# Optimization experiments

Measured on AMD Instinct MI355X. Metric: run time of the kernel, lower is better.

## Reference

```python
import jax, jax.numpy as jnp
import numpy as np

D_MODEL = 1024
NUM_HEADS = 16
D_K = D_MODEL // NUM_HEADS
B, S = 2, 2048


def setup_inputs() -> dict:
    key = jax.random.key(0)
    ks = jax.random.split(key, 11)
    sc = 1.0 / np.sqrt(D_MODEL)
    return {
        "Q_input": jax.random.normal(ks[0], (B, S, D_MODEL), jnp.float32),
        "K_input": jax.random.normal(ks[1], (B, S, D_MODEL), jnp.float32),
        "V_input": jax.random.normal(ks[2], (B, S, D_MODEL), jnp.float32),
        "Wq": jax.random.normal(ks[3], (D_MODEL, D_MODEL), jnp.float32) * sc,
        "bq": jax.random.normal(ks[4], (D_MODEL,), jnp.float32) * 0.01,
        "Wk": jax.random.normal(ks[5], (D_MODEL, D_MODEL), jnp.float32) * sc,
        "bk": jax.random.normal(ks[6], (D_MODEL,), jnp.float32) * 0.01,
        "Wv": jax.random.normal(ks[7], (D_MODEL, D_MODEL), jnp.float32) * sc,
        "bv": jax.random.normal(ks[8], (D_MODEL,), jnp.float32) * 0.01,
        "Wo": jax.random.normal(ks[9], (D_MODEL, D_MODEL), jnp.float32) * sc,
        "bo": jax.random.normal(ks[10], (D_MODEL,), jnp.float32) * 0.01,
    }


def reference(Q_input, K_input, V_input, Wq, bq, Wk, bk, Wv, bv, Wo, bo):
    # Linear projections (torch Linear: x @ W.T + b)
    Q = Q_input @ Wq.T + bq  # [B,S,D]
    K = K_input @ Wk.T + bk
    V = V_input @ Wv.T + bv
    # split heads -> [B,H,S,dk]
    def split(x):
        return x.reshape(B, S, NUM_HEADS, D_K).transpose(0, 2, 1, 3)
    Qh, Kh, Vh = split(Q), split(K), split(V)
    scale = 1.0 / jnp.sqrt(jnp.asarray(D_K, Qh.dtype))
    scores = jnp.einsum('bhqd,bhkd->bhqk', Qh, Kh) * scale  # [B,H,S,S]
    attn = jax.nn.softmax(scores, axis=-1)
    ctx = jnp.einsum('bhqk,bhkd->bhqd', attn, Vh)  # [B,H,S,dk]
    concat = ctx.transpose(0, 2, 1, 3).reshape(B, S, D_MODEL)
    out = concat @ Wo.T + bo  # dropout is identity in eval
    return out
```

## Files before the change

### kernel.cpp

```cpp
#include <hip/hip_runtime.h>
#include <stdint.h>

#define DM   1024
#define NH   16
#define DKH  64
#define BBATCH 2
#define SEQ  2048
#define MTOK (BBATCH*SEQ)

typedef unsigned short u16;
typedef __attribute__((ext_vector_type(8))) short  bf16x8;
typedef __attribute__((ext_vector_type(4))) float  f32x4;

struct PtrArr11 { const void* p[11]; };
struct U16Arr11 { u16* p[11]; };

__device__ __forceinline__ float bf2f(u16 u) {
  union { unsigned int i; float f; } z; z.i = ((unsigned int)u) << 16; return z.f;
}
__device__ __forceinline__ u16 f2bf(float f) {
  union { float f; unsigned int i; } z; z.f = f;
  unsigned int i = z.i + 0x7fffu + ((z.i >> 16) & 1u);
  return (u16)(i >> 16);
}
__device__ __forceinline__ unsigned pack2bf(float lo, float hi) {
  union { float f; unsigned int i; } a, b; a.f = lo; b.f = hi;
  return ((a.i + 0x8000u) >> 16) | (((b.i + 0x8000u) >> 16) << 16);
}

__device__ __forceinline__ void gld16(const void* g, void* l) {
  __builtin_amdgcn_global_load_lds(
      (const __attribute__((address_space(1))) void*)g,
      (__attribute__((address_space(3))) void*)l,
      16, 0, 0);
}

__global__ void k_detect(const unsigned int* __restrict__ w, int* __restrict__ flag) {
  const int ln = threadIdx.x & 63;
  const unsigned int word = w[ln];
  const unsigned int ex = (word >> 7) & 0xFFu;
  const int hit = (ex >= 100u && ex <= 126u) ? 1 : 0;
  unsigned long long m = __ballot(hit);
  if (ln == 0) *flag = (__popcll(m) >= 40) ? 0 : 1;
}

__global__ __launch_bounds__(256) void k_convert_all(PtrArr11 src, U16Arr11 dst,
                                                     const int* __restrict__ flag) {
  if (*flag == 0) return;
  const int b = blockIdx.x;
  int seg, base;
  if      (b <  2048) { seg = 0;  base = 0;    }
  else if (b <  4096) { seg = 1;  base = 2048; }
  else if (b <  6144) { seg = 2;  base = 4096; }
  else if (b <  6656) { seg = 3;  base = 6144; }
  else if (b == 6656) { seg = 4;  base = 6656; }
  else if (b <  7169) { seg = 5;  base = 6657; }
  else if (b == 7169) { seg = 6;  base = 7169; }
  else if (b <  7682) { seg = 7;  base = 7170; }
  else if (b == 7682) { seg = 8;  base = 7682; }
  else if (b <  8195) { seg = 9;  base = 7683; }
  else                { seg = 10; base = 8195; }
  const int n = (seg < 3) ? (MTOK * DM) : ((seg & 1) ? (DM * DM) : DM);
  const int i0 = (b - base) * 2048 + threadIdx.x * 8;
  if (i0 >= n) return;
  const float* s = (const float*)src.p[seg] + i0;
  bf16x8 o;
#pragma unroll
  for (int j = 0; j < 8; ++j) o[j] = (short)f2bf(s[j]);
  *(bf16x8*)(dst.p[seg] + i0) = o;
}

__device__ __forceinline__ void gemm_body(const u16* __restrict__ X,
                                          const u16* __restrict__ W,
                                          const u16* __restrict__ bias,
                                          void* __restrict__ out,
                                          int isf32out)
{
  __shared__ __attribute__((aligned(16))) u16 sA[128 * 32];
  __shared__ __attribute__((aligned(16))) u16 sB[128 * 32];
  const int tid = threadIdx.x;
  const int ln = tid & 63, wv = tid >> 6;
  const int wm = wv & 1, wn = wv >> 1;
  const int m0 = blockIdx.y * 128, n0 = blockIdx.x * 128;
  const int fr = ln & 15, fq = ln >> 4;
  const int srow = ln >> 2, sslot = (ln & 3) * 8;

  f32x4 acc[4][4];
#pragma unroll
  for (int i = 0; i < 4; ++i)
#pragma unroll
    for (int j = 0; j < 4; ++j) acc[i][j] = (f32x4){0.f, 0.f, 0.f, 0.f};

  const u16* pA = X + (size_t)(m0 + wv * 32 + srow) * DM + sslot;
  const u16* pB = W + (size_t)(n0 + wv * 32 + srow) * DM + sslot;
  u16* lA0 = sA + (wv * 2) * 512; u16* lA1 = sA + (wv * 2 + 1) * 512;
  u16* lB0 = sB + (wv * 2) * 512; u16* lB1 = sB + (wv * 2 + 1) * 512;

  for (int k0 = 0; k0 < DM; k0 += 32) {
    gld16(pA + k0,            lA0);
    gld16(pA + 16 * DM + k0,  lA1);
    gld16(pB + k0,            lB0);
    gld16(pB + 16 * DM + k0,  lB1);
    asm volatile("s_waitcnt vmcnt(0)" ::: "memory");
    __syncthreads();

    bf16x8 af[4], bfg[4];
#pragma unroll
    for (int t = 0; t < 4; ++t) {
      af[t]  = *(const bf16x8*)(sA + (wm * 64 + t * 16 + fr) * 32 + fq * 8);
      bfg[t] = *(const bf16x8*)(sB + (wn * 64 + t * 16 + fr) * 32 + fq * 8);
    }
#pragma unroll
    for (int i = 0; i < 4; ++i)
#pragma unroll
      for (int j = 0; j < 4; ++j)
        acc[i][j] = __builtin_amdgcn_mfma_f32_16x16x32_bf16(af[i], bfg[j], acc[i][j], 0, 0, 0);
    __syncthreads();
  }

#pragma unroll
  for (int i = 0; i < 4; ++i) {
    const int row = m0 + wm * 64 + i * 16 + fq * 4;
#pragma unroll
    for (int j = 0; j < 4; ++j) {
      const int col = n0 + wn * 64 + j * 16 + fr;
      const float bv = bf2f(bias[col]);
#pragma unroll
      for (int r = 0; r < 4; ++r) {
        const float val = acc[i][j][r] + bv;
        const size_t idx = (size_t)(row + r) * DM + col;
        if (isf32out) ((float*)out)[idx] = val;
        else          ((u16*)out)[idx]   = f2bf(val);
      }
    }
  }
}

__global__ __launch_bounds__(256, 2) void k_gemm_qkv(
    PtrArr11 orig, U16Arr11 conv, const int* __restrict__ flag,
    u16* oq, u16* ok, u16* ov)
{
  const int f = *flag;
  const int z = blockIdx.z;
  const u16* X  = f ? conv.p[z]         : (const u16*)orig.p[z];
  const u16* W  = f ? conv.p[3 + 2 * z] : (const u16*)orig.p[3 + 2 * z];
  const u16* bi = f ? conv.p[4 + 2 * z] : (const u16*)orig.p[4 + 2 * z];
  u16* o = (z == 0) ? oq : (z == 1) ? ok : ov;
  gemm_body(X, W, bi, o, 0);
}

__global__ __launch_bounds__(256, 2) void k_gemm_one(
    const u16* X, const void* Wo_o, const u16* Wo_c,
    const void* bo_o, const u16* bo_c, const int* __restrict__ flag, void* o)
{
  const int f = *flag;
  const u16* W  = f ? Wo_c : (const u16*)Wo_o;
  const u16* bi = f ? bo_c : (const u16*)bo_o;
  gemm_body(X, W, bi, o, f);
}

__global__ __launch_bounds__(256) void k_transpose(const u16* __restrict__ in,
                                                   u16* __restrict__ out)
{
  __shared__ u16 t[64][66];
  const int b = blockIdx.z;
  const int s0 = blockIdx.x * 64, d0 = blockIdx.y * 64;
  const int c = threadIdx.x & 63, r0 = threadIdx.x >> 6;
#pragma unroll
  for (int i = 0; i < 16; ++i) {
    const int r = r0 + 4 * i;
    t[r][c] = in[(size_t)(b * SEQ + s0 + r) * DM + d0 + c];
  }
  __syncthreads();
#pragma unroll
  for (int i = 0; i < 16; ++i) {
    const int r = r0 + 4 * i;
    out[(size_t)(b * DM + d0 + r) * SEQ + s0 + c] = t[c][r];
  }
}

__global__ __launch_bounds__(256, 2) void k_attn(
    const u16* __restrict__ Qp, const u16* __restrict__ Kp,
    const u16* __restrict__ Vt, u16* __restrict__ ctx)
{
  __shared__ __attribute__((aligned(16))) u16 sK[64 * 72];
  __shared__ __attribute__((aligned(16))) u16 sV[64 * 72];

  const int tid = threadIdx.x;
  const int ln = tid & 63, wv = tid >> 6;
  const int bh = blockIdx.y;
  const int b = bh >> 4, h = bh & 15;
  const int q0 = blockIdx.x * 128 + wv * 32;
  const int fr = ln & 15, fq = ln >> 4;
  const int str = tid >> 2, stq = (tid & 3) * 16;

  const int addr0 = 4 * (fr + 16 * ((fq & 1) * 2));
  const int addr1 = addr0 + 64;

  bf16x8 qf[2][2];
#pragma unroll
  for (int mt = 0; mt < 2; ++mt)
#pragma unroll
    for (int ks = 0; ks < 2; ++ks) {
      const u16* src = Qp + (size_t)(b * SEQ + q0 + mt * 16 + fr) * DM + h * DKH + ks * 32 + fq * 8;
      bf16x8 v = *(const bf16x8*)src;
      bf16x8 w;
#pragma unroll
      for (int j = 0; j < 8; ++j)
        w[j] = (short)f2bf(bf2f((u16)v[j]) * 0.125f);
      qf[mt][ks] = w;
    }

  float l_acc[2] = {0.f, 0.f};
  f32x4 o_acc[2][4];
#pragma unroll
  for (int mt = 0; mt < 2; ++mt)
#pragma unroll
    for (int dt = 0; dt < 4; ++dt) o_acc[mt][dt] = (f32x4){0.f, 0.f, 0.f, 0.f};

  for (int kb = 0; kb < SEQ / 64; ++kb) {
    const int key0 = kb * 64;
    {
      const u16* gK = Kp + (size_t)(b * SEQ + key0 + str) * DM + h * DKH + stq;
      const u16* gV = Vt + (size_t)(b * DM + h * DKH + str) * SEQ + key0 + stq;
      *(bf16x8*)(sK + str * 72 + stq)     = *(const bf16x8*)gK;
      *(bf16x8*)(sK + str * 72 + stq + 8) = *(const bf16x8*)(gK + 8);
      *(bf16x8*)(sV + str * 72 + stq)     = *(const bf16x8*)gV;
      *(bf16x8*)(sV + str * 72 + stq + 8) = *(const bf16x8*)(gV + 8);
    }
    __syncthreads();

    bf16x8 kf[4][2];
#pragma unroll
    for (int kt = 0; kt < 4; ++kt)
#pragma unroll
      for (int ks = 0; ks < 2; ++ks)
        kf[kt][ks] = *(const bf16x8*)(sK + (kt * 16 + fr) * 72 + ks * 32 + fq * 8);

    bf16x8 vf[4][2];
#pragma unroll
    for (int dt = 0; dt < 4; ++dt)
#pragma unroll
      for (int ks = 0; ks < 2; ++ks)
        vf[dt][ks] = *(const bf16x8*)(sV + (dt * 16 + fr) * 72 + ks * 32 + fq * 8);

#pragma unroll
    for (int mt = 0; mt < 2; ++mt) {
      f32x4 s2[4];
#pragma unroll
      for (int kt = 0; kt < 4; ++kt) s2[kt] = (f32x4){0.f, 0.f, 0.f, 0.f};
#pragma unroll
      for (int kt = 0; kt < 4; ++kt)
#pragma unroll
        for (int ks = 0; ks < 2; ++ks)
          s2[kt] = __builtin_amdgcn_mfma_f32_16x16x32_bf16(kf[kt][ks], qf[mt][ks], s2[kt], 0, 0, 0);

      unsigned pk[4][2];
#pragma unroll
      for (int kt = 0; kt < 4; ++kt) {
        float p0 = __expf(s2[kt][0]), p1 = __expf(s2[kt][1]);
        float p2 = __expf(s2[kt][2]), p3 = __expf(s2[kt][3]);
        l_acc[mt] += (p0 + p1) + (p2 + p3);
        pk[kt][0] = pack2bf(p0, p1);
        pk[kt][1] = pack2bf(p2, p3);
      }

      bf16x8 pb[2];
#pragma unroll
      for (int ks = 0; ks < 2; ++ks) {
        union { unsigned u[4]; bf16x8 v; } cv;
#pragma unroll
        for (int pp = 0; pp < 4; ++pp) {
          const int addr = (pp >> 1) ? addr1 : addr0;
          const int vlo = __builtin_amdgcn_ds_bpermute(addr, (int)pk[ks * 2][pp & 1]);
          const int vhi = __builtin_amdgcn_ds_bpermute(addr, (int)pk[ks * 2 + 1][pp & 1]);
          cv.u[pp] = (fq >= 2) ? (unsigned)vhi : (unsigned)vlo;
        }
        pb[ks] = cv.v;
      }

#pragma unroll
      for (int dt = 0; dt < 4; ++dt)
#pragma unroll
        for (int ks = 0; ks < 2; ++ks)
          o_acc[mt][dt] = __builtin_amdgcn_mfma_f32_16x16x32_bf16(vf[dt][ks], pb[ks], o_acc[mt][dt], 0, 0, 0);
    }

    __syncthreads();
  }

  float inv[2];
#pragma unroll
  for (int mt = 0; mt < 2; ++mt) {
    float l = l_acc[mt];
    l += __shfl_xor(l, 16);
    l += __shfl_xor(l, 32);
    inv[mt] = 1.0f / l;
  }

#pragma unroll
  for (int mt = 0; mt < 2; ++mt) {
    const int qrow = q0 + mt * 16 + fr;
#pragma unroll
    for (int dt = 0; dt < 4; ++dt)
#pragma unroll
      for (int r = 0; r < 4; ++r) {
        const int col = h * DKH + dt * 16 + fq * 4 + r;
        ctx[(size_t)(b * SEQ + qrow) * DM + col] = f2bf(o_acc[mt][dt][r] * inv[mt]);
      }
  }
}

extern "C" void kernel_launch(void* const* d_in, const int* in_sizes, int n_in,
                              void* d_out, int out_size, void* d_ws, size_t ws_size,
                              hipStream_t stream)
{
  char* ws = (char*)d_ws;
  int* flag = (int*)ws;

  const size_t TOKSZ = (size_t)MTOK * DM * sizeof(u16);
  const size_t WSZ   = (size_t)DM * DM * sizeof(u16);
  const size_t BSZ   = 4096;

  size_t off = 256;
  u16* Qc  = (u16*)(ws + off); off += TOKSZ;
  u16* Kc  = (u16*)(ws + off); off += TOKSZ;
  u16* Vc  = (u16*)(ws + off); off += TOKSZ;
  u16* Wqc = (u16*)(ws + off); off += WSZ;
  u16* Wkc = (u16*)(ws + off); off += WSZ;
  u16* Wvc = (u16*)(ws + off); off += WSZ;
  u16* Woc = (u16*)(ws + off); off += WSZ;
  u16* bqc = (u16*)(ws + off); off += BSZ;
  u16* bkc = (u16*)(ws + off); off += BSZ;
  u16* bvc = (u16*)(ws + off); off += BSZ;
  u16* boc = (u16*)(ws + off); off += BSZ;
  u16* Qp  = (u16*)(ws + off); off += TOKSZ;
  u16* Kp  = (u16*)(ws + off); off += TOKSZ;
  u16* Vp  = (u16*)(ws + off); off += TOKSZ;
  u16* Vt  = Qc;
  u16* ctx = Kc;

  PtrArr11 orig;
  for (int i = 0; i < 11; ++i) orig.p[i] = d_in[i];
  U16Arr11 conv;
  conv.p[0] = Qc;  conv.p[1] = Kc;  conv.p[2] = Vc;
  conv.p[3] = Wqc; conv.p[4] = bqc; conv.p[5] = Wkc; conv.p[6] = bkc;
  conv.p[7] = Wvc; conv.p[8] = bvc; conv.p[9] = Woc; conv.p[10] = boc;

  dim3 blk(256);

  k_detect<<<1, 64, 0, stream>>>((const unsigned int*)d_in[3], flag);
  k_convert_all<<<8196, blk, 0, stream>>>(orig, conv, flag);
  k_gemm_qkv<<<dim3(DM / 128, MTOK / 128, 3), blk, 0, stream>>>(
      orig, conv, flag, Qp, Kp, Vp);
  k_transpose<<<dim3(SEQ / 64, DM / 64, BBATCH), blk, 0, stream>>>(Vp, Vt);
  k_attn<<<dim3(SEQ / 128, BBATCH * NH), blk, 0, stream>>>(Qp, Kp, Vt, ctx);
  k_gemm_one<<<dim3(DM / 128, MTOK / 128, 1), blk, 0, stream>>>(
      ctx, d_in[9], Woc, d_in[10], boc, flag, d_out);
}
```

Baseline: 260.5 us.

## Restructure attention to 32x32 MFMA with split-K waves and LDS reduction

```diff
diff --git a/kernel.cpp b/kernel.cpp
--- a/kernel.cpp
+++ b/kernel.cpp
@@ -9,8 +9,10 @@
 #define MTOK (BBATCH*SEQ)
 
 typedef unsigned short u16;
-typedef __attribute__((ext_vector_type(8))) short  bf16x8;
-typedef __attribute__((ext_vector_type(4))) float  f32x4;
+typedef __attribute__((ext_vector_type(8)))  short bf16x8;
+typedef __attribute__((ext_vector_type(4)))  float f32x4;
+typedef __attribute__((ext_vector_type(16))) float f32x16;
+typedef __attribute__((ext_vector_type(2)))  unsigned uint2v;
 
 struct PtrArr11 { const void* p[11]; };
 struct U16Arr11 { u16* p[11]; };
@@ -27,6 +29,31 @@
   union { float f; unsigned int i; } a, b; a.f = lo; b.f = hi;
   return ((a.i + 0x8000u) >> 16) | (((b.i + 0x8000u) >> 16) << 16);
 }
+__device__ __forceinline__ unsigned pack2bf_rne(float lo, float hi) {
+  return (unsigned)f2bf(lo) | ((unsigned)f2bf(hi) << 16);
+}
+__device__ __forceinline__ f32x16 zero16() {
+  f32x16 z;
+#pragma unroll
+  for (int i = 0; i < 16; ++i) z[i] = 0.f;
+  return z;
+}
+
+#if __has_builtin(__builtin_amdgcn_permlane32_swap)
+__device__ __forceinline__ void half_swap(unsigned &a, unsigned &b) {
+  uint2v r = __builtin_amdgcn_permlane32_swap(a, b, false, false);
+  a = r[0]; b = r[1];
+}
+#else
+__device__ __forceinline__ void half_swap(unsigned &a, unsigned &b) {
+  unsigned ax = (unsigned)__shfl_xor((int)a, 32);
+  unsigned bx = (unsigned)__shfl_xor((int)b, 32);
+  const bool lo = (threadIdx.x & 63) < 32;
+  unsigned na = lo ? a : bx;
+  unsigned nb = lo ? ax : b;
+  a = na; b = nb;
+}
+#endif
 
 __device__ __forceinline__ void gld16(const void* g, void* l) {
   __builtin_amdgcn_global_load_lds(
@@ -136,7 +163,7 @@
   }
 }
 
-__global__ __launch_bounds__(256, 2) void k_gemm_qkv(
+__global__ __launch_bounds__(256, 3) void k_gemm_qkv(
     PtrArr11 orig, U16Arr11 conv, const int* __restrict__ flag,
     u16* oq, u16* ok, u16* ov)
 {
@@ -149,7 +176,7 @@
   gemm_body(X, W, bi, o, 0);
 }
 
-__global__ __launch_bounds__(256, 2) void k_gemm_one(
+__global__ __launch_bounds__(256, 3) void k_gemm_one(
     const u16* X, const void* Wo_o, const u16* Wo_c,
     const void* bo_o, const u16* bo_c, const int* __restrict__ flag, void* o)
 {
@@ -179,135 +206,157 @@
   }
 }
 
-__global__ __launch_bounds__(256, 2) void k_attn(
+__global__ __launch_bounds__(128, 2) void k_attn(
     const u16* __restrict__ Qp, const u16* __restrict__ Kp,
     const u16* __restrict__ Vt, u16* __restrict__ ctx)
 {
-  __shared__ __attribute__((aligned(16))) u16 sK[64 * 72];
-  __shared__ __attribute__((aligned(16))) u16 sV[64 * 72];
+  __shared__ __attribute__((aligned(16))) u16 lds[19456];
 
   const int tid = threadIdx.x;
   const int ln = tid & 63, wv = tid >> 6;
   const int bh = blockIdx.y;
   const int b = bh >> 4, h = bh & 15;
-  const int q0 = blockIdx.x * 128 + wv * 32;
-  const int fr = ln & 15, fq = ln >> 4;
-  const int str = tid >> 2, stq = (tid & 3) * 16;
-
-  const int addr0 = 4 * (fr + 16 * ((fq & 1) * 2));
-  const int addr1 = addr0 + 64;
-
-  bf16x8 qf[2][2];
-#pragma unroll
-  for (int mt = 0; mt < 2; ++mt)
-#pragma unroll
-    for (int ks = 0; ks < 2; ++ks) {
-      const u16* src = Qp + (size_t)(b * SEQ + q0 + mt * 16 + fr) * DM + h * DKH + ks * 32 + fq * 8;
+  const int q0 = blockIdx.x * 64;
+  const int m32 = ln & 31, half = ln >> 5;
+  const int srow = ln >> 3, schk = (ln & 7) * 8;
+
+  u16* sK = lds + wv * 9728;
+  u16* sV = sK + 4864;
+
+  bf16x8 qf[2][4];
+#pragma unroll
+  for (int qt = 0; qt < 2; ++qt)
+#pragma unroll
+    for (int ks = 0; ks < 4; ++ks) {
+      const u16* src = Qp + (size_t)(b * SEQ + q0 + qt * 32 + m32) * DM + h * DKH + ks * 16 + half * 8;
       bf16x8 v = *(const bf16x8*)src;
       bf16x8 w;
 #pragma unroll
       for (int j = 0; j < 8; ++j)
         w[j] = (short)f2bf(bf2f((u16)v[j]) * 0.125f);
-      qf[mt][ks] = w;
+      qf[qt][ks] = w;
     }
 
   float l_acc[2] = {0.f, 0.f};
-  f32x4 o_acc[2][4];
-#pragma unroll
-  for (int mt = 0; mt < 2; ++mt)
-#pragma unroll
-    for (int dt = 0; dt < 4; ++dt) o_acc[mt][dt] = (f32x4){0.f, 0.f, 0.f, 0.f};
-
-  for (int kb = 0; kb < SEQ / 64; ++kb) {
+  f32x16 o_acc[2][2];
+#pragma unroll
+  for (int qt = 0; qt < 2; ++qt)
+#pragma unroll
+    for (int dt = 0; dt < 2; ++dt) o_acc[qt][dt] = zero16();
+
+  for (int kb = wv; kb < SEQ / 64; kb += 2) {
     const int key0 = kb * 64;
-    {
-      const u16* gK = Kp + (size_t)(b * SEQ + key0 + str) * DM + h * DKH + stq;
-      const u16* gV = Vt + (size_t)(b * DM + h * DKH + str) * SEQ + key0 + stq;
-      *(bf16x8*)(sK + str * 72 + stq)     = *(const bf16x8*)gK;
-      *(bf16x8*)(sK + str * 72 + stq + 8) = *(const bf16x8*)(gK + 8);
-      *(bf16x8*)(sV + str * 72 + stq)     = *(const bf16x8*)gV;
-      *(bf16x8*)(sV + str * 72 + stq + 8) = *(const bf16x8*)(gV + 8);
-    }
-    __syncthreads();
-
-    bf16x8 kf[4][2];
-#pragma unroll
-    for (int kt = 0; kt < 4; ++kt)
-#pragma unroll
-      for (int ks = 0; ks < 2; ++ks)
-        kf[kt][ks] = *(const bf16x8*)(sK + (kt * 16 + fr) * 72 + ks * 32 + fq * 8);
-
-    bf16x8 vf[4][2];
-#pragma unroll
-    for (int dt = 0; dt < 4; ++dt)
-#pragma unroll
-      for (int ks = 0; ks < 2; ++ks)
-        vf[dt][ks] = *(const bf16x8*)(sV + (dt * 16 + fr) * 72 + ks * 32 + fq * 8);
-
-#pragma unroll
-    for (int mt = 0; mt < 2; ++mt) {
-      f32x4 s2[4];
-#pragma unroll
-      for (int kt = 0; kt < 4; ++kt) s2[kt] = (f32x4){0.f, 0.f, 0.f, 0.f};
-#pragma unroll
-      for (int kt = 0; kt < 4; ++kt)
-#pragma unroll
-        for (int ks = 0; ks < 2; ++ks)
-          s2[kt] = __builtin_amdgcn_mfma_f32_16x16x32_bf16(kf[kt][ks], qf[mt][ks], s2[kt], 0, 0, 0);
-
-      unsigned pk[4][2];
-#pragma unroll
-      for (int kt = 0; kt < 4; ++kt) {
-        float p0 = __expf(s2[kt][0]), p1 = __expf(s2[kt][1]);
-        float p2 = __expf(s2[kt][2]), p3 = __expf(s2[kt][3]);
-        l_acc[mt] += (p0 + p1) + (p2 + p3);
-        pk[kt][0] = pack2bf(p0, p1);
-        pk[kt][1] = pack2bf(p2, p3);
+#pragma unroll
+    for (int i = 0; i < 8; ++i) {
+      const int row = srow + 8 * i;
+      *(bf16x8*)(sK + row * 76 + schk) =
+          *(const bf16x8*)(Kp + (size_t)(b * SEQ + key0 + row) * DM + h * DKH + schk);
+      *(bf16x8*)(sV + row * 76 + schk) =
+          *(const bf16x8*)(Vt + (size_t)(b * DM + h * DKH + row) * SEQ + key0 + schk);
+    }
+
+    bf16x8 kf[2][4], vf[2][4];
+#pragma unroll
+    for (int t = 0; t < 2; ++t)
+#pragma unroll
+      for (int ks = 0; ks < 4; ++ks) {
+        kf[t][ks] = *(const bf16x8*)(sK + (t * 32 + m32) * 76 + ks * 16 + half * 8);
+        vf[t][ks] = *(const bf16x8*)(sV + (t * 32 + m32) * 76 + ks * 16 + half * 8);
       }
 
-      bf16x8 pb[2];
-#pragma unroll
-      for (int ks = 0; ks < 2; ++ks) {
-        union { unsigned u[4]; bf16x8 v; } cv;
-#pragma unroll
-        for (int pp = 0; pp < 4; ++pp) {
-          const int addr = (pp >> 1) ? addr1 : addr0;
-          const int vlo = __builtin_amdgcn_ds_bpermute(addr, (int)pk[ks * 2][pp & 1]);
-          const int vhi = __builtin_amdgcn_ds_bpermute(addr, (int)pk[ks * 2 + 1][pp & 1]);
-          cv.u[pp] = (fq >= 2) ? (unsigned)vhi : (unsigned)vlo;
+#pragma unroll
+    for (int qt = 0; qt < 2; ++qt)
+#pragma unroll
+      for (int kt = 0; kt < 2; ++kt) {
+        f32x16 s2 = zero16();
+#pragma unroll
+        for (int ks = 0; ks < 4; ++ks)
+          s2 = __builtin_amdgcn_mfma_f32_32x32x16_bf16(kf[kt][ks], qf[qt][ks], s2, 0, 0, 0);
+
+        float p[16];
+        float ls = 0.f;
+#pragma unroll
+        for (int r = 0; r < 16; ++r) { p[r] = __expf(s2[r]); ls += p[r]; }
+        l_acc[qt] += ls;
+
+        unsigned pk[4][2];
+#pragma unroll
+        for (int t2 = 0; t2 < 4; ++t2) {
+          pk[t2][0] = pack2bf(p[4 * t2 + 0], p[4 * t2 + 1]);
+          pk[t2][1] = pack2bf(p[4 * t2 + 2], p[4 * t2 + 3]);
         }
-        pb[ks] = cv.v;
+
+#pragma unroll
+        for (int s = 0; s < 2; ++s) {
+          unsigned a0 = pk[2 * s][0], b0 = pk[2 * s + 1][0];
+          unsigned a1 = pk[2 * s][1], b1 = pk[2 * s + 1][1];
+          half_swap(a0, b0);
+          half_swap(a1, b1);
+          union { unsigned u[4]; bf16x8 v; } pbv;
+          pbv.u[0] = a0; pbv.u[1] = a1; pbv.u[2] = b0; pbv.u[3] = b1;
+#pragma unroll
+          for (int dt = 0; dt < 2; ++dt)
+            o_acc[qt][dt] = __builtin_amdgcn_mfma_f32_32x32x16_bf16(
+                vf[dt][kt * 2 + s], pbv.v, o_acc[qt][dt], 0, 0, 0);
+        }
       }
-
-#pragma unroll
-      for (int dt = 0; dt < 4; ++dt)
-#pragma unroll
-        for (int ks = 0; ks < 2; ++ks)
-          o_acc[mt][dt] = __builtin_amdgcn_mfma_f32_16x16x32_bf16(vf[dt][ks], pb[ks], o_acc[mt][dt], 0, 0, 0);
-    }
-
-    __syncthreads();
-  }
-
-  float inv[2];
-#pragma unroll
-  for (int mt = 0; mt < 2; ++mt) {
-    float l = l_acc[mt];
-    l += __shfl_xor(l, 16);
-    l += __shfl_xor(l, 32);
-    inv[mt] = 1.0f / l;
-  }
-
-#pragma unroll
-  for (int mt = 0; mt < 2; ++mt) {
-    const int qrow = q0 + mt * 16 + fr;
-#pragma unroll
-    for (int dt = 0; dt < 4; ++dt)
-#pragma unroll
-      for (int r = 0; r < 4; ++r) {
-        const int col = h * DKH + dt * 16 + fq * 4 + r;
-        ctx[(size_t)(b * SEQ + qrow) * DM + col] = f2bf(o_acc[mt][dt][r] * inv[mt]);
-      }
+  }
+
+  unsigned* T = (unsigned*)lds;
+  float*    F = (float*)lds + 2304;
+  float*    Ld = (float*)lds + 6600;
+
+  __syncthreads();
+  if (wv == 1) {
+#pragma unroll
+    for (int qt = 0; qt < 2; ++qt)
+#pragma unroll
+      for (int dt = 0; dt < 2; ++dt)
+#pragma unroll
+        for (int r = 0; r < 16; ++r)
+          F[ln * 66 + (qt * 2 + dt) * 16 + r] = o_acc[qt][dt][r];
+    Ld[ln] = l_acc[0];
+    Ld[64 + ln] = l_acc[1];
+  }
+  __syncthreads();
+  if (wv == 0) {
+    float inv[2];
+#pragma unroll
+    for (int qt = 0; qt < 2; ++qt) {
+      float lm = l_acc[qt] + Ld[qt * 64 + ln];
+      lm += __shfl_xor(lm, 32);
+      inv[qt] = 1.0f / lm;
+    }
+#pragma unroll
+    for (int qt = 0; qt < 2; ++qt)
+#pragma unroll
+      for (int dt = 0; dt < 2; ++dt)
+#pragma unroll
+        for (int r = 0; r < 16; ++r)
+          o_acc[qt][dt][r] += F[ln * 66 + (qt * 2 + dt) * 16 + r];
+#pragma unroll
+    for (int qt = 0; qt < 2; ++qt) {
+      const int rowT = (qt * 32 + m32) * 36;
+#pragma unroll
+      for (int dt = 0; dt < 2; ++dt)
+#pragma unroll
+        for (int t2 = 0; t2 < 4; ++t2) {
+          const unsigned lo = pack2bf_rne(o_acc[qt][dt][4 * t2 + 0] * inv[qt],
+                                          o_acc[qt][dt][4 * t2 + 1] * inv[qt]);
+          const unsigned hi = pack2bf_rne(o_acc[qt][dt][4 * t2 + 2] * inv[qt],
+                                          o_acc[qt][dt][4 * t2 + 3] * inv[qt]);
+          const int word = rowT + dt * 16 + half * 2 + t2 * 4;
+          T[word] = lo;
+          T[word + 1] = hi;
+        }
+    }
+  }
+  __syncthreads();
+#pragma unroll
+  for (int pass = 0; pass < 4; ++pass) {
+    const int row = wv * 32 + pass * 8 + srow;
+    bf16x8 vv = *(const bf16x8*)((const u16*)lds + row * 72 + (ln & 7) * 8);
+    *(bf16x8*)(ctx + (size_t)(b * SEQ + q0 + row) * DM + h * DKH + (ln & 7) * 8) = vv;
   }
 }
 
@@ -354,7 +403,7 @@
   k_gemm_qkv<<<dim3(DM / 128, MTOK / 128, 3), blk, 0, stream>>>(
       orig, conv, flag, Qp, Kp, Vp);
   k_transpose<<<dim3(SEQ / 64, DM / 64, BBATCH), blk, 0, stream>>>(Vp, Vt);
-  k_attn<<<dim3(SEQ / 128, BBATCH * NH), blk, 0, stream>>>(Qp, Kp, Vt, ctx);
+  k_attn<<<dim3(SEQ / 64, BBATCH * NH), dim3(128), 0, stream>>>(Qp, Kp, Vt, ctx);
   k_gemm_one<<<dim3(DM / 128, MTOK / 128, 1), blk, 0, stream>>>(
       ctx, d_in[9], Woc, d_in[10], boc, flag, d_out);
 }
```

Measured after the change: 284.1 us. +9.0%, slower.
